# Performance work log

Measured on AMD Instinct MI355X. Metric: run time of the kernel, lower is better.

Reference implementation:

```python
import jax, jax.numpy as jnp
import numpy as np

B, S, E = 2, 2048, 1024
H = 16
D = E // H  # 64
SCALE = D ** -0.5


def setup_inputs() -> dict:
    key = jax.random.key(0)
    ks = jax.random.split(key, 9)
    w = lambda k: jax.random.normal(k, (E, E), dtype=jnp.float32) * 0.02
    b = lambda k: jax.random.normal(k, (E,), dtype=jnp.float32) * 0.02
    return {
        "hidden_states": jax.random.normal(ks[0], (B, S, E), dtype=jnp.float32),
        "q_w": w(ks[1]), "q_b": b(ks[2]),
        "k_w": w(ks[3]), "k_b": b(ks[4]),
        "v_w": w(ks[5]), "v_b": b(ks[6]),
        "o_w": w(ks[7]), "o_b": b(ks[8]),
    }


def reference(hidden_states, q_w, q_b, k_w, k_b, v_w, v_b, o_w, o_b):
    dtype = hidden_states.dtype
    # torch Linear: y = x @ W^T + b
    q = hidden_states @ q_w.T + q_b
    k = hidden_states @ k_w.T + k_b
    v = hidden_states @ v_w.T + v_b
    # [B,S,E] -> [B*H, S, D]
    split = lambda t: t.reshape(B, S, H, D).transpose(0, 2, 1, 3).reshape(B * H, S, D)
    q, k, v = split(q), split(k), split(v)
    # upcast_attention: fp32 QK^T, scaled (baddbmm with beta=0, no mask)
    scores = SCALE * jnp.einsum("bqd,bkd->bqk", q.astype(jnp.float32), k.astype(jnp.float32))
    # upcast_softmax: fp32 softmax over last dim (transpose_qk=False), cast back
    probs = jax.nn.softmax(scores, axis=-1).astype(dtype)
    # PV bmm, merge heads, out_proj (dropout p=0.0 -> identity)
    out = jnp.einsum("bqk,bkd->bqd", probs, v)
    out = out.reshape(B, H, S, D).transpose(0, 2, 1, 3).reshape(B, S, E)
    return out @ o_w.T + o_b
```

## Files before the change

### kernel.cpp

```cpp
#include <hip/hip_runtime.h>

typedef __bf16 bf16x8 __attribute__((ext_vector_type(8)));
typedef __bf16 bf16x4 __attribute__((ext_vector_type(4)));
typedef float  f32x4  __attribute__((ext_vector_type(4)));

#define CS 0.18033688011112042f

__device__ __forceinline__ float fast_exp2(float x) {
    return __builtin_amdgcn_exp2f(x);
}

__device__ __forceinline__ f32x4 MFMA(bf16x8 a, bf16x8 b, f32x4 c) {
    return __builtin_amdgcn_mfma_f32_16x16x32_bf16(a, b, c, 0, 0, 0);
}

__device__ __forceinline__ void ldsgcpy16(__bf16* lds, const __bf16* g) {
    __builtin_amdgcn_global_load_lds(
        (const __attribute__((address_space(1))) unsigned int*)g,
        (__attribute__((address_space(3))) unsigned int*)lds, 16, 0, 0);
}

__global__ __launch_bounds__(256) void cvt5_kernel(
    const float* __restrict__ s0, const float* __restrict__ s1,
    const float* __restrict__ s2, const float* __restrict__ s3,
    const float* __restrict__ s4,
    __bf16* __restrict__ d0, __bf16* __restrict__ d1, __bf16* __restrict__ d2,
    __bf16* __restrict__ d3, __bf16* __restrict__ d4)
{
    int blk = blockIdx.x;
    const float* src; __bf16* dst; int base;
    if (blk < 4096)      { src = s0; dst = d0; base = blk; }
    else if (blk < 5120) { src = s1; dst = d1; base = blk - 4096; }
    else if (blk < 6144) { src = s2; dst = d2; base = blk - 5120; }
    else if (blk < 7168) { src = s3; dst = d3; base = blk - 6144; }
    else                 { src = s4; dst = d4; base = blk - 7168; }
    int i = base * 1024 + threadIdx.x * 4;
    float4 v = *(const float4*)(src + i);
    bf16x4 o;
    o[0] = (__bf16)v.x; o[1] = (__bf16)v.y; o[2] = (__bf16)v.z; o[3] = (__bf16)v.w;
    *(bf16x4*)(dst + i) = o;
}

template <typename OutT>
__device__ __forceinline__ void gemm_core(const __bf16* __restrict__ A,
                                          const __bf16* __restrict__ W,
                                          const float* __restrict__ bias,
                                          OutT* __restrict__ C,
                                          int m0, int n0, bool vtrans)
{
    __shared__ __bf16 As[128 * 64];
    __shared__ __bf16 Bs[128 * 64];

    const int tid  = threadIdx.x;
    const int lane = tid & 63;
    const int w    = tid >> 6;
    const int wm   = w & 1;
    const int wn   = w >> 1;
    const int s    = lane & 15;
    const int q    = lane >> 4;

    f32x4 acc[4][4];
#pragma unroll
    for (int i = 0; i < 4; i++)
#pragma unroll
        for (int j = 0; j < 4; j++)
#pragma unroll
            for (int r = 0; r < 4; r++) acc[i][j][r] = 0.0f;

    for (int k0 = 0; k0 < 1024; k0 += 64) {
        __syncthreads();
#pragma unroll
        for (int t = 0; t < 4; t++) {
            int c   = tid + 256 * t;
            int row = c >> 3;
            int ccp = (c & 7) ^ (row & 7);
            ldsgcpy16(&As[c * 8], A + (size_t)(m0 + row) * 1024 + k0 + ccp * 8);
            ldsgcpy16(&Bs[c * 8], W + (size_t)(n0 + row) * 1024 + k0 + ccp * 8);
        }
        __syncthreads();

#pragma unroll
        for (int kk = 0; kk < 2; kk++) {
            bf16x8 af[4], bf[4];
#pragma unroll
            for (int i = 0; i < 4; i++) {
                int row = wm * 64 + i * 16 + s;
                int idx = row * 64 + ((((kk << 2) + q) ^ (row & 7)) << 3);
                af[i] = *(const bf16x8*)&As[idx];
            }
#pragma unroll
            for (int j = 0; j < 4; j++) {
                int row = wn * 64 + j * 16 + s;
                int idx = row * 64 + ((((kk << 2) + q) ^ (row & 7)) << 3);
                bf[j] = *(const bf16x8*)&Bs[idx];
            }
#pragma unroll
            for (int i = 0; i < 4; i++)
#pragma unroll
                for (int j = 0; j < 4; j++)
                    acc[i][j] = MFMA(af[i], bf[j], acc[i][j]);
        }
    }

    if (vtrans) {
        __bf16* Vt = (__bf16*)C;
#pragma unroll
        for (int j = 0; j < 4; j++) {
            int col = n0 + wn * 64 + j * 16 + s;
            int h   = col >> 6;
            int d   = col & 63;
            float bv = bias[col];
#pragma unroll
            for (int i = 0; i < 4; i++) {
                int rowb = m0 + wm * 64 + i * 16 + q * 4;
                int b    = rowb >> 11;
                int srow = rowb & 2047;
                bf16x4 pk;
#pragma unroll
                for (int r = 0; r < 4; r++) pk[r] = (__bf16)(acc[i][j][r] + bv);
                *(bf16x4*)&Vt[(size_t)((b * 16 + h) * 64 + d) * 2048 + srow] = pk;
            }
        }
    } else {
#pragma unroll
        for (int j = 0; j < 4; j++) {
            int col = n0 + wn * 64 + j * 16 + s;
            float bv = bias[col];
#pragma unroll
            for (int i = 0; i < 4; i++) {
                int rowb = m0 + wm * 64 + i * 16 + q * 4;
#pragma unroll
                for (int r = 0; r < 4; r++) {
                    C[(size_t)(rowb + r) * 1024 + col] = (OutT)(acc[i][j][r] + bv);
                }
            }
        }
    }
}

__global__ __launch_bounds__(256) void gemm_qkv_kernel(
    const __bf16* __restrict__ X,
    const __bf16* __restrict__ Wq, const float* __restrict__ bq,
    const __bf16* __restrict__ Wk, const float* __restrict__ bk,
    const __bf16* __restrict__ Wv, const float* __restrict__ bv,
    __bf16* __restrict__ Q, __bf16* __restrict__ K, __bf16* __restrict__ Vt)
{
    int mt = blockIdx.x / 24;
    int nt = blockIdx.x % 24;
    int which = nt >> 3;
    const __bf16* W    = (which == 0) ? Wq : (which == 1) ? Wk : Wv;
    const float*  bias = (which == 0) ? bq : (which == 1) ? bk : bv;
    __bf16*       Out  = (which == 0) ? Q  : (which == 1) ? K  : Vt;
    gemm_core<__bf16>(X, W, bias, Out, mt * 128, (nt & 7) * 128, which == 2);
}

__global__ __launch_bounds__(256) void gemm_o_kernel(
    const __bf16* __restrict__ Ain, const __bf16* __restrict__ Wo,
    const float* __restrict__ bo, float* __restrict__ Out)
{
    int mt = blockIdx.x >> 3;
    int nt = blockIdx.x & 7;
    gemm_core<float>(Ain, Wo, bo, Out, mt * 128, nt * 128, false);
}

__global__ __launch_bounds__(256, 2) void attn_kernel(
    const __bf16* __restrict__ Q, const __bf16* __restrict__ K,
    const __bf16* __restrict__ Vt, __bf16* __restrict__ O)
{
    __shared__ __bf16 k_lds[128 * 64];
    __shared__ __bf16 vt_lds[64 * 128];
    __shared__ __bf16 p_lds[4 * 32 * 128];

    const int bh = blockIdx.x >> 4;
    const int qt = blockIdx.x & 15;
    const int b  = bh >> 4;
    const int h  = bh & 15;

    const int tid  = threadIdx.x;
    const int lane = tid & 63;
    const int w    = tid >> 6;
    const int s    = lane & 15;
    const int q    = lane >> 4;

    bf16x8 aq[2][2];
#pragma unroll
    for (int i = 0; i < 2; i++)
#pragma unroll
        for (int kd = 0; kd < 2; kd++) {
            int row = qt * 128 + w * 32 + i * 16 + s;
            aq[i][kd] = *(const bf16x8*)(Q + (size_t)(b * 2048 + row) * 1024 +
                                         h * 64 + kd * 32 + q * 8);
        }

    f32x4 acc_o[2][4];
    float lst[2][4];
#pragma unroll
    for (int i = 0; i < 2; i++)
#pragma unroll
        for (int r = 0; r < 4; r++) {
            lst[i][r] = 0.0f;
#pragma unroll
            for (int jd = 0; jd < 4; jd++) acc_o[i][jd][r] = 0.0f;
        }

    const int pbase = w * 32 * 128;

    bf16x8 kpre[4], vpre[4];
#pragma unroll
    for (int t = 0; t < 4; t++) {
        int c = tid + 256 * t;
        int krow = c >> 3, cc = c & 7;
        kpre[t] = *(const bf16x8*)(K + (size_t)(b * 2048 + krow) * 1024 +
                                   h * 64 + cc * 8);
        int d = c >> 4, ck = c & 15;
        vpre[t] = *(const bf16x8*)(Vt + (size_t)(bh * 64 + d) * 2048 + ck * 8);
    }

    for (int kc = 0; kc < 16; kc++) {
        __syncthreads();
#pragma unroll
        for (int t = 0; t < 4; t++) {
            int c = tid + 256 * t;
            int krow = c >> 3, cc = c & 7;
            *(bf16x8*)&k_lds[krow * 64 + ((cc ^ (krow & 7)) << 3)] = kpre[t];
            int d = c >> 4, ck = c & 15;
            *(bf16x8*)&vt_lds[(d * 16 + (ck ^ (d & 7))) << 3] = vpre[t];
        }
        __syncthreads();

        int kb2 = ((kc + 1) & 15) * 128;
#pragma unroll
        for (int t = 0; t < 4; t++) {
            int c = tid + 256 * t;
            int krow = c >> 3, cc = c & 7;
            kpre[t] = *(const bf16x8*)(K + (size_t)(b * 2048 + kb2 + krow) * 1024 +
                                       h * 64 + cc * 8);
            int d = c >> 4, ck = c & 15;
            vpre[t] = *(const bf16x8*)(Vt + (size_t)(bh * 64 + d) * 2048 + kb2 + ck * 8);
        }

        f32x4 sc[2][8];
#pragma unroll
        for (int i = 0; i < 2; i++)
#pragma unroll
            for (int j = 0; j < 8; j++)
#pragma unroll
                for (int r = 0; r < 4; r++) sc[i][j][r] = 0.0f;
#pragma unroll
        for (int kd = 0; kd < 2; kd++) {
#pragma unroll
            for (int j = 0; j < 8; j++) {
                int row = j * 16 + s;
                int idx = row * 64 + ((((kd << 2) + q) ^ (row & 7)) << 3);
                bf16x8 bf = *(const bf16x8*)&k_lds[idx];
                sc[0][j] = MFMA(aq[0][kd], bf, sc[0][j]);
                sc[1][j] = MFMA(aq[1][kd], bf, sc[1][j]);
            }
        }

#pragma unroll
        for (int i = 0; i < 2; i++)
#pragma unroll
            for (int r = 0; r < 4; r++) {
                int prow = i * 16 + q * 4 + r;
                float rsum = 0.0f;
#pragma unroll
                for (int j = 0; j < 8; j++) {
                    float p = fast_exp2(sc[i][j][r] * CS);
                    rsum += p;
                    int col = j * 16 + s;
                    int idx = pbase + prow * 128 +
                              (((col >> 3) ^ (prow & 7)) << 3) + (col & 7);
                    p_lds[idx] = (__bf16)p;
                }
                lst[i][r] += rsum;
            }

#pragma unroll
        for (int kk = 0; kk < 4; kk++) {
            bf16x8 ap[2];
#pragma unroll
            for (int i = 0; i < 2; i++) {
                int prow = i * 16 + s;
                int aidx = pbase + prow * 128 + ((((kk << 2) + q) ^ (s & 7)) << 3);
                ap[i] = *(const bf16x8*)&p_lds[aidx];
            }
#pragma unroll
            for (int jd = 0; jd < 4; jd++) {
                int d    = jd * 16 + s;
                int vidx = (d * 16 + (((kk << 2) + q) ^ (d & 7))) << 3;
                bf16x8 bv = *(const bf16x8*)&vt_lds[vidx];
                acc_o[0][jd] = MFMA(ap[0], bv, acc_o[0][jd]);
                acc_o[1][jd] = MFMA(ap[1], bv, acc_o[1][jd]);
            }
        }
    }

#pragma unroll
    for (int i = 0; i < 2; i++)
#pragma unroll
        for (int r = 0; r < 4; r++) {
#pragma unroll
            for (int off = 1; off < 16; off <<= 1)
                lst[i][r] += __shfl_xor(lst[i][r], off);
        }

#pragma unroll
    for (int i = 0; i < 2; i++)
#pragma unroll
        for (int jd = 0; jd < 4; jd++)
#pragma unroll
            for (int r = 0; r < 4; r++) {
                int row = qt * 128 + w * 32 + i * 16 + q * 4 + r;
                int col = h * 64 + jd * 16 + s;
                float v = acc_o[i][jd][r] / lst[i][r];
                O[(size_t)(b * 2048 + row) * 1024 + col] = (__bf16)v;
            }
}

extern "C" void kernel_launch(void* const* d_in, const int* in_sizes, int n_in,
                              void* d_out, int out_size, void* d_ws, size_t ws_size,
                              hipStream_t stream)
{
    const float* hs = (const float*)d_in[0];
    const float* qw = (const float*)d_in[1];
    const float* qb = (const float*)d_in[2];
    const float* kw = (const float*)d_in[3];
    const float* kb = (const float*)d_in[4];
    const float* vw = (const float*)d_in[5];
    const float* vb = (const float*)d_in[6];
    const float* ow = (const float*)d_in[7];
    const float* ob = (const float*)d_in[8];
    float* out = (float*)d_out;

    char* ws = (char*)d_ws;
    const size_t MB = (size_t)1024 * 1024;
    __bf16* Xb  = (__bf16*)(ws);
    __bf16* Wqb = (__bf16*)(ws +  8 * MB);
    __bf16* Wkb = (__bf16*)(ws + 10 * MB);
    __bf16* Wvb = (__bf16*)(ws + 12 * MB);
    __bf16* Wob = (__bf16*)(ws + 14 * MB);
    __bf16* Qb  = (__bf16*)(ws + 16 * MB);
    __bf16* Kb  = (__bf16*)(ws + 24 * MB);
    __bf16* Vtb = (__bf16*)(ws + 32 * MB);
    __bf16* Ab  = (__bf16*)(ws + 40 * MB);

    cvt5_kernel<<<dim3(8192), dim3(256), 0, stream>>>(hs, qw, kw, vw, ow,
                                                      Xb, Wqb, Wkb, Wvb, Wob);

    gemm_qkv_kernel<<<dim3(768), dim3(256), 0, stream>>>(Xb, Wqb, qb, Wkb, kb, Wvb, vb,
                                                         Qb, Kb, Vtb);
    attn_kernel<<<dim3(512), dim3(256), 0, stream>>>(Qb, Kb, Vtb, Ab);
    gemm_o_kernel<<<dim3(256), dim3(256), 0, stream>>>(Ab, Wob, ob, out);
}
```

Measured before the change: 215.3 us.

## Permute K/P LDS layout for vector P stores and narrow O-proj tile

Three changes. The attention kernel now permutes K rows in LDS so that each lane's eight score columns become a contiguous P chunk. That lets P be written with one 16-byte store per row instead of eight scalar bf16 stores, using an XOR swizzle over 16 chunks. The output projection GEMM is templated on BN and switched to 128x64 tiles, giving 512 blocks instead of 256 for better CU occupancy on the small N dimension, at the cost of lower per-block reuse.

Measured after the change: 201.0 us. 6.6% less time.

```diff
diff --git a/kernel.cpp b/kernel.cpp
--- a/kernel.cpp
+++ b/kernel.cpp
@@ -41,15 +41,16 @@
     *(bf16x4*)(dst + i) = o;
 }
 
-template <typename OutT>
+template <typename OutT, int BN>
 __device__ __forceinline__ void gemm_core(const __bf16* __restrict__ A,
                                           const __bf16* __restrict__ W,
                                           const float* __restrict__ bias,
                                           OutT* __restrict__ C,
                                           int m0, int n0, bool vtrans)
 {
+    constexpr int NJ = BN / 32;
     __shared__ __bf16 As[128 * 64];
-    __shared__ __bf16 Bs[128 * 64];
+    __shared__ __bf16 Bs[BN * 64];
 
     const int tid  = threadIdx.x;
     const int lane = tid & 63;
@@ -59,11 +60,11 @@
     const int s    = lane & 15;
     const int q    = lane >> 4;
 
-    f32x4 acc[4][4];
+    f32x4 acc[4][NJ];
 #pragma unroll
     for (int i = 0; i < 4; i++)
 #pragma unroll
-        for (int j = 0; j < 4; j++)
+        for (int j = 0; j < NJ; j++)
 #pragma unroll
             for (int r = 0; r < 4; r++) acc[i][j][r] = 0.0f;
 
@@ -75,13 +76,19 @@
             int row = c >> 3;
             int ccp = (c & 7) ^ (row & 7);
             ldsgcpy16(&As[c * 8], A + (size_t)(m0 + row) * 1024 + k0 + ccp * 8);
+        }
+#pragma unroll
+        for (int t = 0; t < BN / 32; t++) {
+            int c   = tid + 256 * t;
+            int row = c >> 3;
+            int ccp = (c & 7) ^ (row & 7);
             ldsgcpy16(&Bs[c * 8], W + (size_t)(n0 + row) * 1024 + k0 + ccp * 8);
         }
         __syncthreads();
 
 #pragma unroll
         for (int kk = 0; kk < 2; kk++) {
-            bf16x8 af[4], bf[4];
+            bf16x8 af[4], bf[NJ];
 #pragma unroll
             for (int i = 0; i < 4; i++) {
                 int row = wm * 64 + i * 16 + s;
@@ -89,15 +96,15 @@
                 af[i] = *(const bf16x8*)&As[idx];
             }
 #pragma unroll
-            for (int j = 0; j < 4; j++) {
-                int row = wn * 64 + j * 16 + s;
+            for (int j = 0; j < NJ; j++) {
+                int row = wn * (BN / 2) + j * 16 + s;
                 int idx = row * 64 + ((((kk << 2) + q) ^ (row & 7)) << 3);
                 bf[j] = *(const bf16x8*)&Bs[idx];
             }
 #pragma unroll
             for (int i = 0; i < 4; i++)
 #pragma unroll
-                for (int j = 0; j < 4; j++)
+                for (int j = 0; j < NJ; j++)
                     acc[i][j] = MFMA(af[i], bf[j], acc[i][j]);
         }
     }
@@ -105,8 +112,8 @@
     if (vtrans) {
         __bf16* Vt = (__bf16*)C;
 #pragma unroll
-        for (int j = 0; j < 4; j++) {
-            int col = n0 + wn * 64 + j * 16 + s;
+        for (int j = 0; j < NJ; j++) {
+            int col = n0 + wn * (BN / 2) + j * 16 + s;
             int h   = col >> 6;
             int d   = col & 63;
             float bv = bias[col];
@@ -123,8 +130,8 @@
         }
     } else {
 #pragma unroll
-        for (int j = 0; j < 4; j++) {
-            int col = n0 + wn * 64 + j * 16 + s;
+        for (int j = 0; j < NJ; j++) {
+            int col = n0 + wn * (BN / 2) + j * 16 + s;
             float bv = bias[col];
 #pragma unroll
             for (int i = 0; i < 4; i++) {
@@ -151,16 +158,16 @@
     const __bf16* W    = (which == 0) ? Wq : (which == 1) ? Wk : Wv;
     const float*  bias = (which == 0) ? bq : (which == 1) ? bk : bv;
     __bf16*       Out  = (which == 0) ? Q  : (which == 1) ? K  : Vt;
-    gemm_core<__bf16>(X, W, bias, Out, mt * 128, (nt & 7) * 128, which == 2);
+    gemm_core<__bf16, 128>(X, W, bias, Out, mt * 128, (nt & 7) * 128, which == 2);
 }
 
 __global__ __launch_bounds__(256) void gemm_o_kernel(
     const __bf16* __restrict__ Ain, const __bf16* __restrict__ Wo,
     const float* __restrict__ bo, float* __restrict__ Out)
 {
-    int mt = blockIdx.x >> 3;
-    int nt = blockIdx.x & 7;
-    gemm_core<float>(Ain, Wo, bo, Out, mt * 128, nt * 128, false);
+    int mt = blockIdx.x >> 4;
+    int nt = blockIdx.x & 15;
+    gemm_core<float, 64>(Ain, Wo, bo, Out, mt * 128, nt * 64, false);
 }
 
 __global__ __launch_bounds__(256, 2) void attn_kernel(
@@ -222,7 +229,8 @@
         for (int t = 0; t < 4; t++) {
             int c = tid + 256 * t;
             int krow = c >> 3, cc = c & 7;
-            *(bf16x8*)&k_lds[krow * 64 + ((cc ^ (krow & 7)) << 3)] = kpre[t];
+            int rho  = ((krow & 7) << 4) | (krow >> 3);
+            *(bf16x8*)&k_lds[rho * 64 + ((cc ^ (rho & 7)) << 3)] = kpre[t];
             int d = c >> 4, ck = c & 15;
             *(bf16x8*)&vt_lds[(d * 16 + (ck ^ (d & 7))) << 3] = vpre[t];
         }
@@ -263,17 +271,17 @@
 #pragma unroll
             for (int r = 0; r < 4; r++) {
                 int prow = i * 16 + q * 4 + r;
+                bf16x8 pk;
                 float rsum = 0.0f;
 #pragma unroll
                 for (int j = 0; j < 8; j++) {
                     float p = fast_exp2(sc[i][j][r] * CS);
                     rsum += p;
-                    int col = j * 16 + s;
-                    int idx = pbase + prow * 128 +
-                              (((col >> 3) ^ (prow & 7)) << 3) + (col & 7);
-                    p_lds[idx] = (__bf16)p;
+                    pk[j] = (__bf16)p;
                 }
                 lst[i][r] += rsum;
+                int chunkp = s ^ (prow & 15);
+                *(bf16x8*)&p_lds[pbase + prow * 128 + (chunkp << 3)] = pk;
             }
 
 #pragma unroll
@@ -282,8 +290,8 @@
 #pragma unroll
             for (int i = 0; i < 2; i++) {
                 int prow = i * 16 + s;
-                int aidx = pbase + prow * 128 + ((((kk << 2) + q) ^ (s & 7)) << 3);
-                ap[i] = *(const bf16x8*)&p_lds[aidx];
+                int chunkr = ((kk << 2) + q) ^ s;
+                ap[i] = *(const bf16x8*)&p_lds[pbase + prow * 128 + (chunkr << 3)];
             }
 #pragma unroll
             for (int jd = 0; jd < 4; jd++) {
@@ -351,5 +359,5 @@
     gemm_qkv_kernel<<<dim3(768), dim3(256), 0, stream>>>(Xb, Wqb, qb, Wkb, kb, Wvb, vb,
                                                          Qb, Kb, Vtb);
     attn_kernel<<<dim3(512), dim3(256), 0, stream>>>(Qb, Kb, Vtb, Ab);
-    gemm_o_kernel<<<dim3(256), dim3(256), 0, stream>>>(Ab, Wob, ob, out);
-}
+    gemm_o_kernel<<<dim3(512), dim3(256), 0, stream>>>(Ab, Wob, ob, out);
+}
```
